# Kernel optimization log

Hardware: AMD Instinct MI355X
Metric: run time of the kernel (lower is better)

## Reference

```python
import jax, jax.numpy as jnp
import numpy as np

N_NODES = 50000
N_EDGES = 800000
FEAT = 128


def setup_inputs() -> dict:
    key = jax.random.key(0)
    k1, k2, k3, k4 = jax.random.split(key, 4)
    x = jax.random.normal(k1, (N_NODES, FEAT), dtype=jnp.float32)
    a = jax.random.normal(k2, (FEAT, 1), dtype=jnp.float32) * (1.414 / np.sqrt(FEAT))
    row = jax.random.randint(k3, (N_EDGES,), 0, N_NODES, dtype=jnp.int64)
    col = jax.random.randint(k4, (N_EDGES,), 0, N_NODES, dtype=jnp.int64)
    return {"x": x, "a": a, "row": row, "col": col}


def reference(x, a, row, col):
    n = x.shape[0]
    # per-node score e = x @ a, squeezed to [N]
    e = jnp.squeeze(x @ a, axis=-1)
    # gather per-edge score from the destination (column) node, as in e[col]
    vals = e[col]                                            # [E]
    # sparse row-wise softmax (numerically stable via segment max)
    m = jax.ops.segment_max(vals, row, num_segments=n)       # [N]
    m = jnp.where(jnp.isfinite(m), m, 0.0)                   # empty rows -> 0
    ex = jnp.exp(vals - m[row])                              # [E]
    denom = jax.ops.segment_sum(ex, row, num_segments=n)     # [N]
    att = ex / denom[row]                                    # [E]
    # sparse-dense matmul: h[i] = sum_j att_ij * x[j]
    h_prime = jax.ops.segment_sum(att[:, None] * x[col], row, num_segments=n)
    return h_prime
```

## Files before the change

### kernel.cpp

```cpp
#include <hip/hip_runtime.h>
#include <hip/hip_bf16.h>
#include <math.h>

#define FEAT 128

__device__ __forceinline__ int pack_bf162(float lo, float hi) {
    __hip_bfloat162 b = __float22bfloat162_rn(make_float2(lo, hi));
    union { __hip_bfloat162 b; int i; } u;
    u.b = b;
    return u.i;
}

__global__ void dot_hist_kernel(const float* __restrict__ x, const float* __restrict__ a,
                                const int* __restrict__ row,
                                float* __restrict__ exw, int* __restrict__ cnt,
                                int2* __restrict__ xh, int n, int nE) {
    int tid = blockIdx.x * blockDim.x + threadIdx.x;
    if (tid < nE) atomicAdd(&cnt[row[tid]], 1);
    int node = tid >> 5;
    int l = tid & 31;
    if (node >= n) return;
    float4 xv = ((const float4*)(x + (size_t)node * FEAT))[l];
    float4 av = ((const float4*)a)[l];
    int2 pk;
    pk.x = pack_bf162(xv.x, xv.y);
    pk.y = pack_bf162(xv.z, xv.w);
    xh[(size_t)node * 32 + l] = pk;
    float p = xv.x * av.x + xv.y * av.y + xv.z * av.z + xv.w * av.w;
    #pragma unroll
    for (int off = 16; off > 0; off >>= 1) p += __shfl_xor(p, off);
    if (l == 0) exw[node] = __expf(p);
}

__global__ void scan_kernel(const int* __restrict__ cnt, int* __restrict__ rowptr,
                            int* __restrict__ cursor, int* flags, int n, int nb) {
    __shared__ int sm[256];
    __shared__ int sprefix;
    int b = blockIdx.x;
    int i0 = (b << 10) + (int)threadIdx.x * 4;
    int v0 = (i0 + 0 < n) ? cnt[i0 + 0] : 0;
    int v1 = (i0 + 1 < n) ? cnt[i0 + 1] : 0;
    int v2 = (i0 + 2 < n) ? cnt[i0 + 2] : 0;
    int v3 = (i0 + 3 < n) ? cnt[i0 + 3] : 0;
    int t4 = v0 + v1 + v2 + v3;
    sm[threadIdx.x] = t4;
    __syncthreads();
    #pragma unroll
    for (int off = 1; off < 256; off <<= 1) {
        int u = (threadIdx.x >= (unsigned)off) ? sm[threadIdx.x - off] : 0;
        __syncthreads();
        sm[threadIdx.x] += u;
        __syncthreads();
    }
    if (threadIdx.x == 0)
        __hip_atomic_store(&flags[b], sm[255] + 1, __ATOMIC_RELEASE,
                           __HIP_MEMORY_SCOPE_AGENT);
    if (threadIdx.x < 64) {
        int lane = threadIdx.x;
        int pred = 0;
        if (lane < b) {
            int f;
            do {
                f = __hip_atomic_load(&flags[lane], __ATOMIC_ACQUIRE,
                                      __HIP_MEMORY_SCOPE_AGENT);
            } while (f == 0);
            pred = f - 1;
        }
        #pragma unroll
        for (int off = 32; off > 0; off >>= 1) pred += __shfl_xor(pred, off);
        if (lane == 0) sprefix = pred;
    }
    __syncthreads();
    int base = sprefix + sm[threadIdx.x] - t4;
    if (i0 + 0 < n) { rowptr[i0 + 0] = base;                cursor[i0 + 0] = base; }
    if (i0 + 1 < n) { rowptr[i0 + 1] = base + v0;           cursor[i0 + 1] = base + v0; }
    if (i0 + 2 < n) { rowptr[i0 + 2] = base + v0 + v1;      cursor[i0 + 2] = base + v0 + v1; }
    if (i0 + 3 < n) { rowptr[i0 + 3] = base + v0 + v1 + v2; cursor[i0 + 3] = base + v0 + v1 + v2; }
    if (b == nb - 1 && threadIdx.x == 255) rowptr[n] = sprefix + sm[255];
}

__global__ void fill_kernel(const int* __restrict__ row, const int* __restrict__ col,
                            int* __restrict__ cursor, unsigned short* __restrict__ ecol,
                            int nE) {
    int k = (blockIdx.x * blockDim.x + threadIdx.x) * 2;
    if (k + 1 < nE) {
        int2 r2 = *(const int2*)(row + k);
        int2 c2 = *(const int2*)(col + k);
        int p0 = atomicAdd(&cursor[r2.x], 1);
        ecol[p0] = (unsigned short)c2.x;
        int p1 = atomicAdd(&cursor[r2.y], 1);
        ecol[p1] = (unsigned short)c2.y;
    } else if (k < nE) {
        int r = row[k], c = col[k];
        int p0 = atomicAdd(&cursor[r], 1);
        ecol[p0] = (unsigned short)c;
    }
}

__global__ void gather_kernel(const __hip_bfloat162* __restrict__ xh,
                              const float* __restrict__ exw,
                              const int* __restrict__ rowptr,
                              const unsigned short* __restrict__ ecol,
                              float* __restrict__ h, int n) {
    __shared__ __align__(16) int2 sbuf[4][64];
    int wid = threadIdx.x >> 6;
    int node = (int)((blockIdx.x * blockDim.x + threadIdx.x) >> 6);
    int lane = threadIdx.x & 63;
    if (node >= n) return;
    int s = rowptr[node];
    int eend = rowptr[node + 1];
    float accx = 0.0f, accy = 0.0f, wsum = 0.0f;
    const int4* sb4 = (const int4*)&sbuf[wid][0];
    for (int base = s; base < eend; base += 64) {
        int idx = base + lane;
        float w = 0.0f;
        if (idx < eend) {
            int c = (int)ecol[idx];
            w = exw[c];
            sbuf[wid][lane] = make_int2(c << 6, __float_as_int(w));
        }
        #pragma unroll
        for (int off = 32; off > 0; off >>= 1) w += __shfl_xor(w, off);
        wsum += w;
        int m = min(64, eend - base);
        int j = 0;
        for (; j + 4 <= m; j += 4) {
            int4 q0 = sb4[(j >> 1) + 0];
            int4 q1 = sb4[(j >> 1) + 1];
            float2 f0 = __bfloat1622float2(xh[q0.x + lane]);
            float2 f1 = __bfloat1622float2(xh[q0.z + lane]);
            float2 f2 = __bfloat1622float2(xh[q1.x + lane]);
            float2 f3 = __bfloat1622float2(xh[q1.z + lane]);
            float w0 = __int_as_float(q0.y), w1 = __int_as_float(q0.w);
            float w2 = __int_as_float(q1.y), w3 = __int_as_float(q1.w);
            accx += w0 * f0.x; accy += w0 * f0.y;
            accx += w1 * f1.x; accy += w1 * f1.y;
            accx += w2 * f2.x; accy += w2 * f2.y;
            accx += w3 * f3.x; accy += w3 * f3.y;
        }
        for (; j < m; ++j) {
            int2 p = sbuf[wid][j];
            float2 f = __bfloat1622float2(xh[p.x + lane]);
            float wj = __int_as_float(p.y);
            accx += wj * f.x; accy += wj * f.y;
        }
    }
    float inv = (eend > s) ? 1.0f / wsum : 0.0f;
    float2 out;
    out.x = accx * inv;
    out.y = accy * inv;
    ((float2*)(h + (size_t)node * FEAT))[lane] = out;
}

extern "C" void kernel_launch(void* const* d_in, const int* in_sizes, int n_in,
                              void* d_out, int out_size, void* d_ws, size_t ws_size,
                              hipStream_t stream) {
    const float* x = (const float*)d_in[0];
    const float* a = (const float*)d_in[1];
    const int* row = (const int*)d_in[2];
    const int* col = (const int*)d_in[3];
    int n  = in_sizes[0] / FEAT;
    int nE = in_sizes[2];
    float* h = (float*)d_out;
    int nb = (n + 1023) / 1024;

    char* p = (char*)d_ws;
    auto alloc = [&](size_t bytes) { char* q = p; p += (bytes + 15) & ~(size_t)15; return q; };
    int* cnt             = (int*)alloc((size_t)n * 4);
    int* flags           = (int*)alloc(64 * 4);
    int* cursor          = (int*)alloc((size_t)n * 4);
    float* exw           = (float*)alloc((size_t)n * 4);
    int* rowptr          = (int*)alloc((size_t)(n + 1) * 4);
    unsigned short* ecol = (unsigned short*)alloc((size_t)nE * 2);
    int2* xh             = (int2*)alloc((size_t)n * 32 * 8);

    hipMemsetAsync(cnt, 0, ((size_t)n + 64) * sizeof(int), stream);

    int t1 = (n * 32 > nE) ? n * 32 : nE;
    dot_hist_kernel<<<(t1 + 255) / 256, 256, 0, stream>>>(x, a, row, exw, cnt, xh, n, nE);
    scan_kernel<<<nb, 256, 0, stream>>>(cnt, rowptr, cursor, flags, n, nb);
    fill_kernel<<<(nE / 2 + 255) / 256, 256, 0, stream>>>(row, col, cursor, ecol, nE);
    gather_kernel<<<(n + 3) / 4, 256, 0, stream>>>((const __hip_bfloat162*)xh, exw,
                                                   rowptr, ecol, h, n);
}
```

Before: 199.5 us.

## Record per-edge rank in histogram and fuse scan with atomic-free fill

The histogram pass now saves each edge's atomicAdd return value as its rank within its row. That lets the CSR fill place edges at rowptr[row]+rank without a second round of atomics on a cursor array. The scan and fill are merged into one persistent kernel of 1024 blocks: the scan blocks publish rowptr, every block spins on a global done counter, and then all blocks do a grid-stride fill. This removes one kernel launch and the contended cursor atomics, at the cost of writing an extra rank array. It also relies on all 1024 blocks being co-resident for the spin barrier to be safe.

```diff
diff --git a/kernel.cpp b/kernel.cpp
--- a/kernel.cpp
+++ b/kernel.cpp
@@ -3,6 +3,7 @@
 #include <math.h>
 
 #define FEAT 128
+#define NF 1024
 
 __device__ __forceinline__ int pack_bf162(float lo, float hi) {
     __hip_bfloat162 b = __float22bfloat162_rn(make_float2(lo, hi));
@@ -13,10 +14,14 @@
 
 __global__ void dot_hist_kernel(const float* __restrict__ x, const float* __restrict__ a,
                                 const int* __restrict__ row,
-                                float* __restrict__ exw, int* __restrict__ cnt,
+                                float* __restrict__ exw, unsigned* __restrict__ cnt,
+                                unsigned short* __restrict__ rank,
                                 int2* __restrict__ xh, int n, int nE) {
     int tid = blockIdx.x * blockDim.x + threadIdx.x;
-    if (tid < nE) atomicAdd(&cnt[row[tid]], 1);
+    if (tid < nE) {
+        unsigned old = atomicAdd(&cnt[row[tid]], 1u);
+        rank[tid] = (unsigned short)old;
+    }
     int node = tid >> 5;
     int l = tid & 31;
     if (node >= n) return;
@@ -32,68 +37,81 @@
     if (l == 0) exw[node] = __expf(p);
 }
 
-__global__ void scan_kernel(const int* __restrict__ cnt, int* __restrict__ rowptr,
-                            int* __restrict__ cursor, int* flags, int n, int nb) {
+__global__ void __launch_bounds__(256) scanfill_kernel(
+    const unsigned* __restrict__ cnt, int* __restrict__ rowptr,
+    const int* __restrict__ row, const int* __restrict__ col,
+    const unsigned short* __restrict__ rank,
+    unsigned short* __restrict__ ecol,
+    unsigned* flags, unsigned* done, int n, int nb, int nE)
+{
     __shared__ int sm[256];
     __shared__ int sprefix;
     int b = blockIdx.x;
-    int i0 = (b << 10) + (int)threadIdx.x * 4;
-    int v0 = (i0 + 0 < n) ? cnt[i0 + 0] : 0;
-    int v1 = (i0 + 1 < n) ? cnt[i0 + 1] : 0;
-    int v2 = (i0 + 2 < n) ? cnt[i0 + 2] : 0;
-    int v3 = (i0 + 3 < n) ? cnt[i0 + 3] : 0;
-    int t4 = v0 + v1 + v2 + v3;
-    sm[threadIdx.x] = t4;
+    if (b < nb) {
+        int i0 = (b << 10) + (int)threadIdx.x * 4;
+        int v0 = (i0 + 0 < n) ? (int)cnt[i0 + 0] : 0;
+        int v1 = (i0 + 1 < n) ? (int)cnt[i0 + 1] : 0;
+        int v2 = (i0 + 2 < n) ? (int)cnt[i0 + 2] : 0;
+        int v3 = (i0 + 3 < n) ? (int)cnt[i0 + 3] : 0;
+        int t4 = v0 + v1 + v2 + v3;
+        sm[threadIdx.x] = t4;
+        __syncthreads();
+        #pragma unroll
+        for (int off = 1; off < 256; off <<= 1) {
+            int u = (threadIdx.x >= (unsigned)off) ? sm[threadIdx.x - off] : 0;
+            __syncthreads();
+            sm[threadIdx.x] += u;
+            __syncthreads();
+        }
+        if (threadIdx.x == 0)
+            __hip_atomic_store(&flags[b], (unsigned)sm[255] + 1u, __ATOMIC_RELEASE,
+                               __HIP_MEMORY_SCOPE_AGENT);
+        if (threadIdx.x < 64) {
+            int lane = threadIdx.x;
+            unsigned pred = 0;
+            if (lane < b) {
+                unsigned f;
+                do {
+                    f = __hip_atomic_load(&flags[lane], __ATOMIC_ACQUIRE,
+                                          __HIP_MEMORY_SCOPE_AGENT);
+                } while (f == 0u);
+                pred = f - 1u;
+            }
+            #pragma unroll
+            for (int off = 32; off > 0; off >>= 1) pred += __shfl_xor(pred, off);
+            if (lane == 0) sprefix = (int)pred;
+        }
+        __syncthreads();
+        int base = sprefix + sm[threadIdx.x] - t4;
+        if (i0 + 0 < n) rowptr[i0 + 0] = base;
+        if (i0 + 1 < n) rowptr[i0 + 1] = base + v0;
+        if (i0 + 2 < n) rowptr[i0 + 2] = base + v0 + v1;
+        if (i0 + 3 < n) rowptr[i0 + 3] = base + v0 + v1 + v2;
+        if (b == nb - 1 && threadIdx.x == 255) rowptr[n] = sprefix + sm[255];
+        __syncthreads();
+        if (threadIdx.x == 0) {
+            __threadfence();
+            __hip_atomic_fetch_add(done, 1u, __ATOMIC_RELEASE,
+                                   __HIP_MEMORY_SCOPE_AGENT);
+        }
+    }
+    if (threadIdx.x == 0) {
+        while (__hip_atomic_load(done, __ATOMIC_ACQUIRE, __HIP_MEMORY_SCOPE_AGENT)
+               < (unsigned)nb)
+            __builtin_amdgcn_s_sleep(8);
+    }
     __syncthreads();
-    #pragma unroll
-    for (int off = 1; off < 256; off <<= 1) {
-        int u = (threadIdx.x >= (unsigned)off) ? sm[threadIdx.x - off] : 0;
-        __syncthreads();
-        sm[threadIdx.x] += u;
-        __syncthreads();
-    }
-    if (threadIdx.x == 0)
-        __hip_atomic_store(&flags[b], sm[255] + 1, __ATOMIC_RELEASE,
-                           __HIP_MEMORY_SCOPE_AGENT);
-    if (threadIdx.x < 64) {
-        int lane = threadIdx.x;
-        int pred = 0;
-        if (lane < b) {
-            int f;
-            do {
-                f = __hip_atomic_load(&flags[lane], __ATOMIC_ACQUIRE,
-                                      __HIP_MEMORY_SCOPE_AGENT);
-            } while (f == 0);
-            pred = f - 1;
-        }
-        #pragma unroll
-        for (int off = 32; off > 0; off >>= 1) pred += __shfl_xor(pred, off);
-        if (lane == 0) sprefix = pred;
-    }
-    __syncthreads();
-    int base = sprefix + sm[threadIdx.x] - t4;
-    if (i0 + 0 < n) { rowptr[i0 + 0] = base;                cursor[i0 + 0] = base; }
-    if (i0 + 1 < n) { rowptr[i0 + 1] = base + v0;           cursor[i0 + 1] = base + v0; }
-    if (i0 + 2 < n) { rowptr[i0 + 2] = base + v0 + v1;      cursor[i0 + 2] = base + v0 + v1; }
-    if (i0 + 3 < n) { rowptr[i0 + 3] = base + v0 + v1 + v2; cursor[i0 + 3] = base + v0 + v1 + v2; }
-    if (b == nb - 1 && threadIdx.x == 255) rowptr[n] = sprefix + sm[255];
-}
-
-__global__ void fill_kernel(const int* __restrict__ row, const int* __restrict__ col,
-                            int* __restrict__ cursor, unsigned short* __restrict__ ecol,
-                            int nE) {
-    int k = (blockIdx.x * blockDim.x + threadIdx.x) * 2;
-    if (k + 1 < nE) {
-        int2 r2 = *(const int2*)(row + k);
-        int2 c2 = *(const int2*)(col + k);
-        int p0 = atomicAdd(&cursor[r2.x], 1);
-        ecol[p0] = (unsigned short)c2.x;
-        int p1 = atomicAdd(&cursor[r2.y], 1);
-        ecol[p1] = (unsigned short)c2.y;
-    } else if (k < nE) {
-        int r = row[k], c = col[k];
-        int p0 = atomicAdd(&cursor[r], 1);
-        ecol[p0] = (unsigned short)c;
+    int gid = b * 256 + (int)threadIdx.x;
+    for (int k = gid * 2; k < nE; k += NF * 512) {
+        if (k + 1 < nE) {
+            int2 r2 = *(const int2*)(row + k);
+            int2 c2 = *(const int2*)(col + k);
+            unsigned rk = *(const unsigned*)(rank + k);
+            ecol[rowptr[r2.x] + (int)(rk & 0xFFFFu)] = (unsigned short)c2.x;
+            ecol[rowptr[r2.y] + (int)(rk >> 16)]     = (unsigned short)c2.y;
+        } else {
+            ecol[rowptr[row[k]] + (int)rank[k]] = (unsigned short)col[k];
+        }
     }
 }
 
@@ -166,20 +184,22 @@
 
     char* p = (char*)d_ws;
     auto alloc = [&](size_t bytes) { char* q = p; p += (bytes + 15) & ~(size_t)15; return q; };
-    int* cnt             = (int*)alloc((size_t)n * 4);
-    int* flags           = (int*)alloc(64 * 4);
-    int* cursor          = (int*)alloc((size_t)n * 4);
+    unsigned* cnt        = (unsigned*)alloc((size_t)n * 4);
+    unsigned* flags      = (unsigned*)alloc(64 * 4);
+    unsigned* done       = (unsigned*)alloc(16 * 4);
     float* exw           = (float*)alloc((size_t)n * 4);
     int* rowptr          = (int*)alloc((size_t)(n + 1) * 4);
+    unsigned short* rank = (unsigned short*)alloc((size_t)nE * 2);
     unsigned short* ecol = (unsigned short*)alloc((size_t)nE * 2);
     int2* xh             = (int2*)alloc((size_t)n * 32 * 8);
 
-    hipMemsetAsync(cnt, 0, ((size_t)n + 64) * sizeof(int), stream);
+    hipMemsetAsync(cnt, 0, ((size_t)n + 80) * sizeof(unsigned), stream);
 
     int t1 = (n * 32 > nE) ? n * 32 : nE;
-    dot_hist_kernel<<<(t1 + 255) / 256, 256, 0, stream>>>(x, a, row, exw, cnt, xh, n, nE);
-    scan_kernel<<<nb, 256, 0, stream>>>(cnt, rowptr, cursor, flags, n, nb);
-    fill_kernel<<<(nE / 2 + 255) / 256, 256, 0, stream>>>(row, col, cursor, ecol, nE);
+    dot_hist_kernel<<<(t1 + 255) / 256, 256, 0, stream>>>(x, a, row, exw, cnt, rank,
+                                                          xh, n, nE);
+    scanfill_kernel<<<NF, 256, 0, stream>>>(cnt, rowptr, row, col, rank, ecol,
+                                            flags, done, n, nb, nE);
     gather_kernel<<<(n + 3) / 4, 256, 0, stream>>>((const __hip_bfloat162*)xh, exw,
                                                    rowptr, ecol, h, n);
 }
```

Result: slower. 213.2 us (+6.9%).
